# Kernel optimization log

Measured on AMD Instinct MI355X. Metric: run time of the kernel, lower is better.

Reference implementation:

```python
import jax, jax.numpy as jnp
import numpy as np

EPS = 1e-5  # torch LayerNorm default
NUM_HEADS = 4


def _ln(x, g, b):
    mu = jnp.mean(x, axis=-1, keepdims=True)
    var = jnp.mean((x - mu) ** 2, axis=-1, keepdims=True)
    return (x - mu) * jax.lax.rsqrt(var + EPS) * g + b


def setup_inputs() -> dict:
    key = jax.random.key(0)
    ks = jax.random.split(key, 12)
    B, nm, A, H, W, E = 1, 64, 8400, 160, 160, 128
    f32 = jnp.float32
    return {
        "coefficients": jax.random.normal(ks[0], (B, nm, A), f32),
        "prototypes": jax.random.normal(ks[1], (B, nm, H, W), f32),
        "q_w": 0.1 * jax.random.normal(ks[2], (E,), f32),
        "q_b": 0.1 * jax.random.normal(ks[3], (E,), f32),
        "q_g": jnp.ones((E,), f32),
        "q_beta": jnp.zeros((E,), f32),
        "k_w": 0.1 * jax.random.normal(ks[4], (E,), f32),
        "k_b": 0.1 * jax.random.normal(ks[5], (E,), f32),
        "k_g": jnp.ones((E,), f32),
        "k_beta": jnp.zeros((E,), f32),
        "v_w": 0.1 * jax.random.normal(ks[6], (E,), f32),
        "v_b": 0.1 * jax.random.normal(ks[7], (E,), f32),
        "v_g": jnp.ones((E,), f32),
        "v_beta": jnp.zeros((E,), f32),
        "out_w": 0.1 * jax.random.normal(ks[8], (E,), f32),
        "out_b": 0.1 * jax.random.normal(ks[9], (), f32),
        "gate_w": 0.1 * jax.random.normal(ks[10], (2,), f32),
        "gate_b": 0.1 * jax.random.normal(ks[11], (), f32),
    }


def reference(coefficients, prototypes, q_w, q_b, q_g, q_beta,
              k_w, k_b, k_g, k_beta, v_w, v_b, v_g, v_beta,
              out_w, out_b, gate_w, gate_b):
    B, nm, A = coefficients.shape
    E = q_w.shape[0]
    h = NUM_HEADS
    d = E // h
    scale = jnp.asarray(d, coefficients.dtype) ** -0.5

    # AdaptiveAvgPool2d(1): global mean over H,W -> (B, nm)
    pooled = jnp.mean(prototypes, axis=(2, 3))

    # per-scalar Linear(1,E) + LayerNorm; keys/values shared across anchors
    keys = _ln(pooled[..., None] * k_w + k_b, k_g, k_beta)      # (B, nm, E)
    values = _ln(pooled[..., None] * v_w + v_b, v_g, v_beta)    # (B, nm, E)
    q_in = jnp.swapaxes(coefficients, 1, 2)                      # (B, A, nm)
    queries = _ln(q_in[..., None] * q_w + q_b, q_g, q_beta)     # (B, A, nm, E)

    q = queries.reshape(B, A, nm, h, d)
    k = keys.reshape(B, nm, h, d)
    v = values.reshape(B, nm, h, d)

    # tiny nm x nm attention per (batch, anchor, head); broadcast K/V over anchors
    scores = jnp.einsum('banhd,bmhd->bahnm', q, k) * scale       # (B, A, h, nm, nm)
    attn = jax.nn.softmax(scores, axis=-1)
    out = jnp.einsum('bahnm,bmhd->banhd', attn, v).reshape(B, A, nm, E)

    # out_proj Linear(E,1)
    refined = jnp.swapaxes(out @ out_w + out_b, 1, 2)            # (B, nm, A)

    # gate: sigmoid(Linear(2,1)([orig, refined]))
    g = jax.nn.sigmoid(coefficients * gate_w[0] + refined * gate_w[1] + gate_b)
    return g * refined + (1.0 - g) * coefficients
```

## Files before the change

### kernel.cpp

```cpp
#include <hip/hip_runtime.h>
#include <math.h>

#define LN_EPS 1e-5f
#define NM 64
#define E_DIM 128
#define NH 4
#define TOTAL 537600
#define SCALE 0.17677669529663687f
#define LOG2E 1.4426950408889634f
#define NPTS 8192
#define XMIN -8.0f
#define XRANGE 16.0f
#define H_STEP (XRANGE / (NPTS - 1))
#define INV_H ((float)(NPTS - 1) / XRANGE)


__global__ __launch_bounds__(256) void pool_kernel(const float* __restrict__ protos,
                                                   float* __restrict__ pool_part) {
    int bx = blockIdx.x;
    int m = bx >> 2, s = bx & 3;
    const float4* p4 = reinterpret_cast<const float4*>(protos + (size_t)m * 25600);
    float acc = 0.f;
    for (int i = s * 1600 + threadIdx.x; i < (s + 1) * 1600; i += 256) {
        float4 v = p4[i];
        acc += (v.x + v.y) + (v.z + v.w);
    }
#pragma unroll
    for (int off = 32; off; off >>= 1) acc += __shfl_down(acc, off);
    __shared__ float w[4];
    if ((threadIdx.x & 63) == 0) w[threadIdx.x >> 6] = acc;
    __syncthreads();
    if (threadIdx.x == 0) pool_part[bx] = (w[0] + w[1]) + (w[2] + w[3]);
}

__device__ inline float block_sum256(float v, float* scratch) {
#pragma unroll
    for (int off = 32; off; off >>= 1) v += __shfl_down(v, off);
    if ((threadIdx.x & 63) == 0) scratch[threadIdx.x >> 6] = v;
    __syncthreads();
    float r = (scratch[0] + scratch[1]) + (scratch[2] + scratch[3]);
    __syncthreads();
    return r;
}

__global__ __launch_bounds__(256) void build_kernel(
    const float* __restrict__ pool_part,
    const float* __restrict__ q_w, const float* __restrict__ q_b,
    const float* __restrict__ q_g, const float* __restrict__ q_beta,
    const float* __restrict__ k_w, const float* __restrict__ k_b,
    const float* __restrict__ k_g, const float* __restrict__ k_beta,
    const float* __restrict__ v_w, const float* __restrict__ v_b,
    const float* __restrict__ v_g, const float* __restrict__ v_beta,
    const float* __restrict__ out_w, const float* __restrict__ out_b,
    float* __restrict__ Ftab) {
    __shared__ float4 tabs[256];
    __shared__ float scratch[4];
    int t = threadIdx.x;
    int m = t >> 2, h = t & 3;

    float lw = (t < E_DIM) ? q_w[t] : 0.f;
    float lb = (t < E_DIM) ? q_b[t] : 0.f;
    float mw = block_sum256(lw, scratch) * (1.0f / E_DIM);
    float mb = block_sum256(lb, scratch) * (1.0f / E_DIM);
    float dw = (t < E_DIM) ? (lw - mw) : 0.f;
    float db = (t < E_DIM) ? (lb - mb) : 0.f;
    float a2 = block_sum256(dw * dw, scratch) * (1.0f / E_DIM);
    float a1 = block_sum256(dw * db, scratch) * (1.0f / E_DIM);
    float a0 = block_sum256(db * db, scratch) * (1.0f / E_DIM);

    float p = pool_part[t];
    p += __shfl_xor(p, 1);
    p += __shfl_xor(p, 2);
    p *= (1.0f / 25600.0f);

    float kin[32], vin[32];
    float sk = 0.f, sv = 0.f;
#pragma unroll
    for (int j = 0; j < 32; ++j) {
        int e = h * 32 + j;
        kin[j] = fmaf(p, k_w[e], k_b[e]);
        vin[j] = fmaf(p, v_w[e], v_b[e]);
        sk += kin[j];
        sv += vin[j];
    }
    sk += __shfl_xor(sk, 1); sk += __shfl_xor(sk, 2);
    sv += __shfl_xor(sv, 1); sv += __shfl_xor(sv, 2);
    float muk = sk * (1.0f / E_DIM), muv = sv * (1.0f / E_DIM);
    float vk = 0.f, vv = 0.f;
#pragma unroll
    for (int j = 0; j < 32; ++j) {
        float dk = kin[j] - muk, dv = vin[j] - muv;
        vk = fmaf(dk, dk, vk);
        vv = fmaf(dv, dv, vv);
    }
    vk += __shfl_xor(vk, 1); vk += __shfl_xor(vk, 2);
    vv += __shfl_xor(vv, 1); vv += __shfl_xor(vv, 2);
    float rk = rsqrtf(vk * (1.0f / E_DIM) + LN_EPS);
    float rv = rsqrtf(vv * (1.0f / E_DIM) + LN_EPS);

    float kc = 0.f, k1 = 0.f, kb = 0.f, vwv = 0.f;
#pragma unroll
    for (int j = 0; j < 32; ++j) {
        int e = h * 32 + j;
        float key = fmaf((kin[j] - muk) * rk, k_g[e], k_beta[e]);
        float val = fmaf((vin[j] - muv) * rv, v_g[e], v_beta[e]);
        kc = fmaf((q_w[e] - mw) * q_g[e], key, kc);
        k1 = fmaf((q_b[e] - mb) * q_g[e], key, k1);
        kb = fmaf(q_beta[e], key, kb);
        vwv = fmaf(val, out_w[e], vwv);
    }
    const float SL = SCALE * LOG2E;
    tabs[h * 64 + m] = make_float4(SL * kc, SL * k1, SL * kb, vwv);
    __syncthreads();

    int jpt = blockIdx.x * 256 + t;
    float x = fmaf((float)jpt, H_STEP, XMIN);
    float var = fmaf(x, fmaf(x, a2, 2.0f * a1), a0);
    float r = rsqrtf(var + LN_EPS);
    float al = r * x, be = r;
    float Fv = out_b[0];
#pragma unroll
    for (int hh = 0; hh < NH; ++hh) {
        const float4* th = tabs + hh * 64;
        float den = 0.f, num = 0.f;
#pragma unroll 8
        for (int mm = 0; mm < NM; ++mm) {
            float4 tv = th[mm];
            float s = fmaf(al, tv.x, fmaf(be, tv.y, tv.z));
            float e = exp2f(s);
            den += e;
            num = fmaf(e, tv.w, num);
        }
        Fv += num / den;
    }
    Ftab[jpt] = Fv;
}

__global__ __launch_bounds__(256) void apply_kernel(
    const float4* __restrict__ coeff4,
    const float* __restrict__ Ftab_g,
    const float* __restrict__ gate_w,
    const float* __restrict__ gate_b,
    float4* __restrict__ out4) {
    __shared__ float Ft[NPTS];
    {
        const float4* F4 = (const float4*)Ftab_g;
        float4* Fs4 = (float4*)Ft;
#pragma unroll
        for (int k = 0; k < NPTS / 4 / 256; ++k)
            Fs4[threadIdx.x + k * 256] = F4[threadIdx.x + k * 256];
    }
    __syncthreads();

    int idx = blockIdx.x * 256 + threadIdx.x;
    float4 c4 = coeff4[idx];
    float c[4] = {c4.x, c4.y, c4.z, c4.w};
    float gw0 = gate_w[0], gw1 = gate_w[1], gb = gate_b[0];
    float o[4];
#pragma unroll
    for (int i = 0; i < 4; ++i) {
        float u = (c[i] - XMIN) * INV_H;
        u = fminf(fmaxf(u, 0.0f), (float)(NPTS - 2));
        float jf = floorf(u);
        int j = (int)jf;
        float f = u - jf;
        float F0 = Ft[j], F1 = Ft[j + 1];
        float Fv = fmaf(f, F1 - F0, F0);
        float z = fmaf(c[i], gw0, fmaf(Fv, gw1, gb));
        float g = 1.0f / (1.0f + __expf(-z));
        o[i] = fmaf(g, Fv - c[i], c[i]);
    }
    out4[idx] = make_float4(o[0], o[1], o[2], o[3]);
}

extern "C" void kernel_launch(void* const* d_in, const int* in_sizes, int n_in,
                              void* d_out, int out_size, void* d_ws, size_t ws_size,
                              hipStream_t stream) {
    const float* coeff   = (const float*)d_in[0];
    const float* protos  = (const float*)d_in[1];
    const float* q_w     = (const float*)d_in[2];
    const float* q_b     = (const float*)d_in[3];
    const float* q_g     = (const float*)d_in[4];
    const float* q_beta  = (const float*)d_in[5];
    const float* k_w     = (const float*)d_in[6];
    const float* k_b     = (const float*)d_in[7];
    const float* k_g     = (const float*)d_in[8];
    const float* k_beta  = (const float*)d_in[9];
    const float* v_w     = (const float*)d_in[10];
    const float* v_b     = (const float*)d_in[11];
    const float* v_g     = (const float*)d_in[12];
    const float* v_beta  = (const float*)d_in[13];
    const float* out_w   = (const float*)d_in[14];
    const float* out_b   = (const float*)d_in[15];
    const float* gate_w  = (const float*)d_in[16];
    const float* gate_b  = (const float*)d_in[17];

    float* ws        = (float*)d_ws;
    float* pool_part = ws;
    float* Ftab      = ws + 256;

    pool_kernel<<<256, 256, 0, stream>>>(protos, pool_part);
    build_kernel<<<NPTS / 256, 256, 0, stream>>>(pool_part,
        q_w, q_b, q_g, q_beta, k_w, k_b, k_g, k_beta,
        v_w, v_b, v_g, v_beta, out_w, out_b, Ftab);
    apply_kernel<<<TOTAL / 4 / 256, 256, 0, stream>>>(
        (const float4*)coeff, Ftab, gate_w, gate_b, (float4*)d_out);
}
```

Measured before the change: 119.4 us.

## Fuse pool, table build and apply into one cooperative kernel with grid syncs

Replaces the three separate launches with one cooperative kernel of 256 blocks. Two grid-wide syncs separate the prototype pooling, the lookup-table build and the gated apply stages. The table build is redistributed so that each block computes 32 points, with 8 threads per point splitting heads and halves of m. The apply stage becomes a grid-stride loop that loads the 32KB table into LDS once per block. The aim is to remove launch gaps and repeated table loads, at the cost of grid-sync overhead and lower parallelism in the apply stage. The old three-kernel path remains as a fallback if the cooperative launch fails.

```diff
diff --git a/kernel.cpp b/kernel.cpp
--- a/kernel.cpp
+++ b/kernel.cpp
@@ -1,5 +1,8 @@
 #include <hip/hip_runtime.h>
+#include <hip/hip_cooperative_groups.h>
 #include <math.h>
+
+namespace cg = cooperative_groups;
 
 #define LN_EPS 1e-5f
 #define NM 64
@@ -13,7 +16,182 @@
 #define XRANGE 16.0f
 #define H_STEP (XRANGE / (NPTS - 1))
 #define INV_H ((float)(NPTS - 1) / XRANGE)
-
+#define GRID 256
+
+
+__device__ __forceinline__ float block_sum256(float v, float* scratch) {
+#pragma unroll
+    for (int off = 32; off; off >>= 1) v += __shfl_down(v, off);
+    if ((threadIdx.x & 63) == 0) scratch[threadIdx.x >> 6] = v;
+    __syncthreads();
+    float r = (scratch[0] + scratch[1]) + (scratch[2] + scratch[3]);
+    __syncthreads();
+    return r;
+}
+
+__global__ __launch_bounds__(256) void fused_kernel(
+    const float* __restrict__ coeff,
+    const float* __restrict__ protos,
+    const float* __restrict__ q_w, const float* __restrict__ q_b,
+    const float* __restrict__ q_g, const float* __restrict__ q_beta,
+    const float* __restrict__ k_w, const float* __restrict__ k_b,
+    const float* __restrict__ k_g, const float* __restrict__ k_beta,
+    const float* __restrict__ v_w, const float* __restrict__ v_b,
+    const float* __restrict__ v_g, const float* __restrict__ v_beta,
+    const float* __restrict__ out_w, const float* __restrict__ out_b,
+    const float* __restrict__ gate_w, const float* __restrict__ gate_b,
+    float* __restrict__ ws,
+    float* __restrict__ outp) {
+    __shared__ float Ft[NPTS];
+    __shared__ float4 tabs[256];
+    __shared__ float scratch[4];
+
+    cg::grid_group grid = cg::this_grid();
+    int t = threadIdx.x;
+    int bx = blockIdx.x;
+
+    float* pool_part = ws;
+    float* Ftab      = ws + 256;
+
+    {
+        int m = bx >> 2, s = bx & 3;
+        const float4* p4 = reinterpret_cast<const float4*>(protos + (size_t)m * 25600);
+        float acc = 0.f;
+        for (int i = s * 1600 + t; i < (s + 1) * 1600; i += 256) {
+            float4 v = p4[i];
+            acc += (v.x + v.y) + (v.z + v.w);
+        }
+#pragma unroll
+        for (int off = 32; off; off >>= 1) acc += __shfl_down(acc, off);
+        if ((t & 63) == 0) scratch[t >> 6] = acc;
+        __syncthreads();
+        if (t == 0) pool_part[bx] = (scratch[0] + scratch[1]) + (scratch[2] + scratch[3]);
+        __syncthreads();
+    }
+
+    float lw = (t < E_DIM) ? q_w[t] : 0.f;
+    float lb = (t < E_DIM) ? q_b[t] : 0.f;
+    float mw = block_sum256(lw, scratch) * (1.0f / E_DIM);
+    float mb = block_sum256(lb, scratch) * (1.0f / E_DIM);
+    float dw = (t < E_DIM) ? (lw - mw) : 0.f;
+    float db = (t < E_DIM) ? (lb - mb) : 0.f;
+    float a2 = block_sum256(dw * dw, scratch) * (1.0f / E_DIM);
+    float a1 = block_sum256(dw * db, scratch) * (1.0f / E_DIM);
+    float a0 = block_sum256(db * db, scratch) * (1.0f / E_DIM);
+
+    grid.sync();
+
+    {
+        int m = t >> 2, h = t & 3;
+
+        float p = pool_part[t];
+        p += __shfl_xor(p, 1);
+        p += __shfl_xor(p, 2);
+        p *= (1.0f / 25600.0f);
+
+        float kin[32], vin[32];
+        float sk = 0.f, sv = 0.f;
+#pragma unroll
+        for (int j = 0; j < 32; ++j) {
+            int e = h * 32 + j;
+            kin[j] = fmaf(p, k_w[e], k_b[e]);
+            vin[j] = fmaf(p, v_w[e], v_b[e]);
+            sk += kin[j];
+            sv += vin[j];
+        }
+        sk += __shfl_xor(sk, 1); sk += __shfl_xor(sk, 2);
+        sv += __shfl_xor(sv, 1); sv += __shfl_xor(sv, 2);
+        float muk = sk * (1.0f / E_DIM), muv = sv * (1.0f / E_DIM);
+        float vk = 0.f, vv = 0.f;
+#pragma unroll
+        for (int j = 0; j < 32; ++j) {
+            float dk = kin[j] - muk, dv = vin[j] - muv;
+            vk = fmaf(dk, dk, vk);
+            vv = fmaf(dv, dv, vv);
+        }
+        vk += __shfl_xor(vk, 1); vk += __shfl_xor(vk, 2);
+        vv += __shfl_xor(vv, 1); vv += __shfl_xor(vv, 2);
+        float rk = rsqrtf(vk * (1.0f / E_DIM) + LN_EPS);
+        float rv = rsqrtf(vv * (1.0f / E_DIM) + LN_EPS);
+
+        float kc = 0.f, k1 = 0.f, kb = 0.f, vwv = 0.f;
+#pragma unroll
+        for (int j = 0; j < 32; ++j) {
+            int e = h * 32 + j;
+            float key = fmaf((kin[j] - muk) * rk, k_g[e], k_beta[e]);
+            float val = fmaf((vin[j] - muv) * rv, v_g[e], v_beta[e]);
+            kc = fmaf((q_w[e] - mw) * q_g[e], key, kc);
+            k1 = fmaf((q_b[e] - mb) * q_g[e], key, k1);
+            kb = fmaf(q_beta[e], key, kb);
+            vwv = fmaf(val, out_w[e], vwv);
+        }
+        const float SL = SCALE * LOG2E;
+        tabs[h * 64 + m] = make_float4(SL * kc, SL * k1, SL * kb, vwv);
+        __syncthreads();
+    }
+
+    {
+        int pt   = t >> 3;
+        int sub  = t & 7;
+        int head = sub >> 1;
+        int half = sub & 1;
+        int jpt = bx * 32 + pt;
+        float x = fmaf((float)jpt, H_STEP, XMIN);
+        float var = fmaf(x, fmaf(x, a2, 2.0f * a1), a0);
+        float r = rsqrtf(var + LN_EPS);
+        float al = r * x, be = r;
+        const float4* th = tabs + head * 64 + half * 32;
+        float den = 0.f, num = 0.f;
+#pragma unroll
+        for (int mm = 0; mm < 32; ++mm) {
+            float4 tv = th[mm];
+            float s = fmaf(al, tv.x, fmaf(be, tv.y, tv.z));
+            float e = exp2f(s);
+            den += e;
+            num = fmaf(e, tv.w, num);
+        }
+        den += __shfl_xor(den, 1);
+        num += __shfl_xor(num, 1);
+        float ratio = num / den;
+        ratio += __shfl_xor(ratio, 2);
+        ratio += __shfl_xor(ratio, 4);
+        if (sub == 0) Ftab[jpt] = out_b[0] + ratio;
+    }
+
+    grid.sync();
+
+    {
+        const float4* F4 = (const float4*)Ftab;
+        float4* Fs4 = (float4*)Ft;
+#pragma unroll
+        for (int k2 = 0; k2 < NPTS / 4 / 256; ++k2)
+            Fs4[t + k2 * 256] = F4[t + k2 * 256];
+        __syncthreads();
+
+        const float4* coeff4 = (const float4*)coeff;
+        float4* out4 = (float4*)outp;
+        float gw0 = gate_w[0], gw1 = gate_w[1], gb = gate_b[0];
+        for (int idx = bx * 256 + t; idx < TOTAL / 4; idx += GRID * 256) {
+            float4 c4 = coeff4[idx];
+            float c[4] = {c4.x, c4.y, c4.z, c4.w};
+            float o[4];
+#pragma unroll
+            for (int i = 0; i < 4; ++i) {
+                float u = (c[i] - XMIN) * INV_H;
+                u = fminf(fmaxf(u, 0.0f), (float)(NPTS - 2));
+                float jf = floorf(u);
+                int j = (int)jf;
+                float f = u - jf;
+                float F0 = Ft[j], F1 = Ft[j + 1];
+                float Fv = fmaf(f, F1 - F0, F0);
+                float z = fmaf(c[i], gw0, fmaf(Fv, gw1, gb));
+                float g = 1.0f / (1.0f + __expf(-z));
+                o[i] = fmaf(g, Fv - c[i], c[i]);
+            }
+            out4[idx] = make_float4(o[0], o[1], o[2], o[3]);
+        }
+    }
+}
 
 __global__ __launch_bounds__(256) void pool_kernel(const float* __restrict__ protos,
                                                    float* __restrict__ pool_part) {
@@ -31,16 +209,6 @@
     if ((threadIdx.x & 63) == 0) w[threadIdx.x >> 6] = acc;
     __syncthreads();
     if (threadIdx.x == 0) pool_part[bx] = (w[0] + w[1]) + (w[2] + w[3]);
-}
-
-__device__ inline float block_sum256(float v, float* scratch) {
-#pragma unroll
-    for (int off = 32; off; off >>= 1) v += __shfl_down(v, off);
-    if ((threadIdx.x & 63) == 0) scratch[threadIdx.x >> 6] = v;
-    __syncthreads();
-    float r = (scratch[0] + scratch[1]) + (scratch[2] + scratch[3]);
-    __syncthreads();
-    return r;
 }
 
 __global__ __launch_bounds__(256) void build_kernel(
@@ -194,15 +362,28 @@
     const float* out_b   = (const float*)d_in[15];
     const float* gate_w  = (const float*)d_in[16];
     const float* gate_b  = (const float*)d_in[17];
-
-    float* ws        = (float*)d_ws;
-    float* pool_part = ws;
-    float* Ftab      = ws + 256;
-
-    pool_kernel<<<256, 256, 0, stream>>>(protos, pool_part);
-    build_kernel<<<NPTS / 256, 256, 0, stream>>>(pool_part,
-        q_w, q_b, q_g, q_beta, k_w, k_b, k_g, k_beta,
-        v_w, v_b, v_g, v_beta, out_w, out_b, Ftab);
-    apply_kernel<<<TOTAL / 4 / 256, 256, 0, stream>>>(
-        (const float4*)coeff, Ftab, gate_w, gate_b, (float4*)d_out);
-}
+    float* ws   = (float*)d_ws;
+    float* outp = (float*)d_out;
+
+    const float* c_coeff = coeff;
+    void* args[] = {
+        (void*)&c_coeff, (void*)&protos,
+        (void*)&q_w, (void*)&q_b, (void*)&q_g, (void*)&q_beta,
+        (void*)&k_w, (void*)&k_b, (void*)&k_g, (void*)&k_beta,
+        (void*)&v_w, (void*)&v_b, (void*)&v_g, (void*)&v_beta,
+        (void*)&out_w, (void*)&out_b, (void*)&gate_w, (void*)&gate_b,
+        (void*)&ws, (void*)&outp,
+    };
+    hipError_t err = hipLaunchCooperativeKernel((const void*)fused_kernel,
+                                                dim3(GRID), dim3(256), args, 0, stream);
+    if (err != hipSuccess) {
+        float* pool_part = ws;
+        float* Ftab      = ws + 256;
+        pool_kernel<<<256, 256, 0, stream>>>(protos, pool_part);
+        build_kernel<<<NPTS / 256, 256, 0, stream>>>(pool_part,
+            q_w, q_b, q_g, q_beta, k_w, k_b, k_g, k_beta,
+            v_w, v_b, v_g, v_beta, out_w, out_b, Ftab);
+        apply_kernel<<<TOTAL / 4 / 256, 256, 0, stream>>>(
+            (const float4*)coeff, Ftab, gate_w, gate_b, (float4*)d_out);
+    }
+}
```

After: 191.7 us. 60.6% more time.
